# Performance work log

Measured on AMD Instinct MI355X. Metric: run time of the kernel, lower is better.

The kernel has to match this reference:

```python
import jax, jax.numpy as jnp
import numpy as np

TAU = 2.0
EPS = 1e-5
T, B, C, H, W = 4, 16, 256, 32, 32
HEADS = 8
HD = C // HEADS
N = H * W


def make_spike(grad_fn):
    @jax.custom_vjp
    def f(x):
        return (x >= 0.0).astype(x.dtype)
    def fwd(x):
        return f(x), x
    def bwd(res, g):
        return (g * grad_fn(res),)
    f.defvjp(fwd, bwd)
    return f

# ATan surrogate (alpha=5.0) used by q/k/v LIF nodes
spike_atan5 = make_spike(lambda x: (5.0 / 2.0) / (1.0 + (jnp.pi / 2.0 * 5.0 * x) ** 2))
# default Sigmoid surrogate (alpha=4.0) for shortcut_lif / talking_heads_lif
def _sig_grad(x):
    s = jax.nn.sigmoid(4.0 * x)
    return 4.0 * s * (1.0 - s)
spike_sig4 = make_spike(_sig_grad)


def lif(x, spike, v_th=1.0):
    # multi-step LIF over leading time axis; hard reset to 0, detach_reset
    def step(v, xt):
        h = v + (xt - v) / TAU
        s = spike(h - v_th)
        v_new = h * (1.0 - jax.lax.stop_gradient(s))
        return v_new, s
    _, out = jax.lax.scan(step, jnp.zeros_like(x[0]), x)
    return out


def conv1x1(x, w):
    # x: (T,B,C,H,W), w: (Cout,Cin) from Conv2d kernel_size=1
    return jnp.einsum('tbchw,oc->tbohw', x, w)


def bn(y, gamma, beta, mean, var):
    scale = (gamma / jnp.sqrt(var + EPS))[None, None, :, None, None]
    shift = (beta - mean * gamma / jnp.sqrt(var + EPS))[None, None, :, None, None]
    return y * scale + shift


def to_heads(x):
    # (T,B,C,H,W) -> (T,B,heads,N,hd); matches flatten(3).transpose(-1,-2).reshape.permute
    x = x.reshape(T, B, C, N).transpose(0, 1, 3, 2)          # (T,B,N,C)
    x = x.reshape(T, B, N, HEADS, HD).transpose(0, 1, 3, 2, 4)  # (T,B,heads,N,hd)
    return x


def setup_inputs() -> dict:
    key = jax.random.key(0)
    ks = jax.random.split(key, 20)
    def bn_params(i):
        return (1.0 + 0.1 * jax.random.normal(ks[i], (C,), jnp.float32),
                0.1 * jax.random.normal(ks[i + 1], (C,), jnp.float32),
                0.1 * jax.random.normal(ks[i + 2], (C,), jnp.float32),
                jax.random.uniform(ks[i + 3], (C,), jnp.float32, 0.5, 1.5))
    q_g, q_b, q_m, q_var = bn_params(1)
    k_g, k_b, k_m, k_var = bn_params(5)
    v_g, v_b, v_m, v_var = bn_params(9)
    p_g, p_b, p_m, p_var = bn_params(13)
    std = 1.0 / np.sqrt(C)
    return {
        'x': jax.random.normal(ks[0], (T, B, C, H, W), jnp.float32),
        'q_w': std * jax.random.normal(ks[17], (C, C), jnp.float32),
        'q_g': q_g, 'q_b': q_b, 'q_m': q_m, 'q_var': q_var,
        'k_w': std * jax.random.normal(ks[18], (C, C), jnp.float32),
        'k_g': k_g, 'k_b': k_b, 'k_m': k_m, 'k_var': k_var,
        'v_w': std * jax.random.normal(ks[19], (C, C), jnp.float32),
        'v_g': v_g, 'v_b': v_b, 'v_m': v_m, 'v_var': v_var,
        'proj_w': std * jax.random.normal(ks[4], (C, C), jnp.float32),
        'proj_bias': 0.01 * jax.random.normal(ks[8], (C,), jnp.float32),
        'p_g': p_g, 'p_b': p_b, 'p_m': p_m, 'p_var': p_var,
    }


def reference(x, q_w, q_g, q_b, q_m, q_var, k_w, k_g, k_b, k_m, k_var,
              v_w, v_g, v_b, v_m, v_var, proj_w, proj_bias, p_g, p_b, p_m, p_var):
    identity = x
    xs = lif(x, spike_sig4, 1.0)                      # shortcut_lif
    q = to_heads(lif(bn(conv1x1(xs, q_w), q_g, q_b, q_m, q_var), spike_atan5, 1.0))
    k = to_heads(lif(bn(conv1x1(xs, k_w), k_g, k_b, k_m, k_var), spike_atan5, 1.0))
    v = to_heads(lif(bn(conv1x1(xs, v_w), v_g, v_b, v_m, v_var), spike_atan5, 1.0))
    kv = jnp.sum(k * v, axis=-2, keepdims=True)       # (T,B,heads,1,hd)
    kv = lif(kv, spike_sig4, 0.5)                     # talking_heads_lif, v_th=0.5
    attn = q * kv                                     # (T,B,heads,N,hd)
    # transpose(3,4).reshape(T,B,C,H,W)
    out = attn.transpose(0, 1, 2, 4, 3).reshape(T, B, C, H, W)
    out = conv1x1(out, proj_w) + proj_bias[None, None, :, None, None]
    out = bn(out, p_g, p_b, p_m, p_var)
    out = out + identity
    return out, v
```

## Files before the change

### kernel.cpp

```cpp
#include <hip/hip_runtime.h>
#include <hip/hip_bf16.h>
#include <stdint.h>

#define T_ 4
#define B_ 16
#define C_ 256
#define N_ 1024
#define HEADS_ 8
#define HD_ 32

typedef unsigned long long u64;
typedef unsigned char u8;

__global__ __launch_bounds__(256) void prep_kernel(
    const float* __restrict__ qw, const float* __restrict__ kw,
    const float* __restrict__ vw, const float* __restrict__ pw,
    const float* __restrict__ qg, const float* __restrict__ qb2,
    const float* __restrict__ qmn, const float* __restrict__ qvr,
    const float* __restrict__ kg, const float* __restrict__ kb2,
    const float* __restrict__ kmn, const float* __restrict__ kvr,
    const float* __restrict__ vg, const float* __restrict__ vb2,
    const float* __restrict__ vmn, const float* __restrict__ vvr,
    const float* __restrict__ pg, const float* __restrict__ pb2,
    const float* __restrict__ pmn, const float* __restrict__ pvr,
    float* __restrict__ wtq, float* __restrict__ wtk,
    float* __restrict__ wtv, float* __restrict__ wtp,
    float* __restrict__ bnt) {
  if (blockIdx.x < 256) {
    int c = blockIdx.x;
    int o = threadIdx.x;
    wtq[c * C_ + o] = qw[o * C_ + c];
    wtk[c * C_ + o] = kw[o * C_ + c];
    wtv[c * C_ + o] = vw[o * C_ + c];
    wtp[c * C_ + o] = pw[o * C_ + c];
  } else {
    int c = threadIdx.x;
    float rs;
    rs = sqrtf(qvr[c] + 1e-5f);
    bnt[0 * C_ + c] = qg[c] / rs;
    bnt[1 * C_ + c] = qb2[c] - qmn[c] * qg[c] / rs;
    rs = sqrtf(kvr[c] + 1e-5f);
    bnt[2 * C_ + c] = kg[c] / rs;
    bnt[3 * C_ + c] = kb2[c] - kmn[c] * kg[c] / rs;
    rs = sqrtf(vvr[c] + 1e-5f);
    bnt[4 * C_ + c] = vg[c] / rs;
    bnt[5 * C_ + c] = vb2[c] - vmn[c] * vg[c] / rs;
    rs = sqrtf(pvr[c] + 1e-5f);
    bnt[6 * C_ + c] = pg[c] / rs;
    bnt[7 * C_ + c] = pb2[c] - pmn[c] * pg[c] / rs;
  }
}

__global__ __launch_bounds__(256) void lif_shortcut(const float* __restrict__ x,
                                                    u64* __restrict__ xsm) {
  int b = blockIdx.x >> 5;
  int n0 = (blockIdx.x & 31) << 5;
  int tid = threadIdx.x;
  int l = tid & 63, w = tid >> 6;
  __shared__ float tile[C_ * 33];
  float v[32];
#pragma unroll
  for (int i = 0; i < 32; i++) v[i] = 0.f;
  int c = (w << 6) + l;
  for (int t = 0; t < T_; t++) {
    __syncthreads();
    const float* xp = x + (((size_t)t * B_ + b) * C_) * N_ + n0;
    for (int idx = tid; idx < C_ * 32; idx += 256) {
      int cc = idx >> 5, nn = idx & 31;
      tile[cc * 33 + nn] = xp[(size_t)cc * N_ + nn];
    }
    __syncthreads();
#pragma unroll
    for (int nn = 0; nn < 32; nn++) {
      float xv = tile[c * 33 + nn];
      float h = v[nn] + (xv - v[nn]) * 0.5f;
      bool s = h >= 1.0f;
      v[nn] = s ? 0.f : h;
      u64 bal = __ballot(s);
      if (l == nn) xsm[(((size_t)t * B_ + b) * N_ + n0 + nn) * 4 + w] = bal;
    }
  }
}

__global__ __launch_bounds__(256) void qkv_sparse(
    const u64* __restrict__ xsm,
    const float* __restrict__ wtq, const float* __restrict__ wtk,
    const float* __restrict__ wtv, const float* __restrict__ bnt,
    float* __restrict__ pkv, u64* __restrict__ qm_out,
    float* __restrict__ vout) {
  int b = blockIdx.x >> 7;
  int nt = blockIdx.x & 127;
  int n0 = nt << 3;
  int tid = threadIdx.x;
  int l = tid & 63, wv = tid >> 6;
  float qs[4], qsh[4], ks[4], ksh[4], vsc[4], vsh[4];
#pragma unroll
  for (int j = 0; j < 4; j++) {
    int o = (j << 6) + l;
    qs[j]  = bnt[0 * C_ + o]; qsh[j] = bnt[1 * C_ + o];
    ks[j]  = bnt[2 * C_ + o]; ksh[j] = bnt[3 * C_ + o];
    vsc[j] = bnt[4 * C_ + o]; vsh[j] = bnt[5 * C_ + o];
  }
  int cnt[4][4];
#pragma unroll
  for (int t = 0; t < 4; t++)
#pragma unroll
    for (int j = 0; j < 4; j++) cnt[t][j] = 0;

  for (int nn = wv; nn < 8; nn += 4) {
    int n = n0 + nn;
    float aq[4][4], ak[4][4], av[4][4];
#pragma unroll
    for (int t = 0; t < 4; t++)
#pragma unroll
      for (int j = 0; j < 4; j++) { aq[t][j] = 0.f; ak[t][j] = 0.f; av[t][j] = 0.f; }
#pragma unroll
    for (int t = 0; t < 4; t++) {
      const u64* mp = xsm + ((((size_t)t * B_ + b) * N_ + n) << 2);
#pragma unroll
      for (int wd = 0; wd < 4; wd++) {
        u64 m = mp[wd];
        while (m) {
          int c = (wd << 6) + __builtin_ctzll(m);
          m &= (m - 1);
          const float* rq = wtq + c * C_;
          const float* rk = wtk + c * C_;
          const float* rv = wtv + c * C_;
#pragma unroll
          for (int j = 0; j < 4; j++) {
            int o = (j << 6) + l;
            aq[t][j] += rq[o];
            ak[t][j] += rk[o];
            av[t][j] += rv[o];
          }
        }
      }
    }
#pragma unroll
    for (int j = 0; j < 4; j++) {
      int o = (j << 6) + l;
      float vq = 0.f, vk = 0.f, vv = 0.f;
#pragma unroll
      for (int t = 0; t < 4; t++) {
        float pq = aq[t][j] * qs[j] + qsh[j];
        float pk = ak[t][j] * ks[j] + ksh[j];
        float pv = av[t][j] * vsc[j] + vsh[j];
        float hq = vq + (pq - vq) * 0.5f;
        float hk = vk + (pk - vk) * 0.5f;
        float hv = vv + (pv - vv) * 0.5f;
        bool sq = hq >= 1.0f; vq = sq ? 0.f : hq;
        bool sk = hk >= 1.0f; vk = sk ? 0.f : hk;
        bool sv = hv >= 1.0f; vv = sv ? 0.f : hv;
        cnt[t][j] += (sk && sv) ? 1 : 0;
        vout[(((size_t)t * B_ + b) * HEADS_ + (o >> 5)) * ((size_t)N_ * HD_) +
             (size_t)n * HD_ + (o & 31)] = sv ? 1.0f : 0.0f;
        u64 bal = __ballot(sq);
        if (l == (t << 2) + j)
          qm_out[((((size_t)t * B_ + b) * N_ + n) << 2) + j] = bal;
      }
    }
  }
  __shared__ int scnt[4][4][C_];
#pragma unroll
  for (int t = 0; t < 4; t++)
#pragma unroll
    for (int j = 0; j < 4; j++) scnt[wv][t][(j << 6) + l] = cnt[t][j];
  __syncthreads();
  for (int idx = tid; idx < 4 * C_; idx += 256) {
    int t = idx >> 8, c = idx & 255;
    int s = scnt[0][t][c] + scnt[1][t][c] + scnt[2][t][c] + scnt[3][t][c];
    pkv[(((size_t)t * B_ + b) * 128 + nt) * C_ + c] = (float)s;
  }
}

__global__ __launch_bounds__(1024) void kv_lif_kernel(const float* __restrict__ pkv,
                                                      u64* __restrict__ kvsm) {
  int b = blockIdx.x;
  int tid = threadIdx.x;
  int c = tid & 255, qtr = tid >> 8;
  __shared__ float part[4][4][C_];
#pragma unroll
  for (int t = 0; t < 4; t++) {
    const float* p = pkv + ((((size_t)t * B_ + b) * 128) + (qtr << 5)) * C_ + c;
    float s = 0.f;
#pragma unroll
    for (int i = 0; i < 32; i++) s += p[(size_t)i * C_];
    part[qtr][t][c] = s;
  }
  __syncthreads();
  if (tid < 256) {
    int l = c & 63, j = c >> 6;
    float v = 0.f;
#pragma unroll
    for (int t = 0; t < 4; t++) {
      float kv = part[0][t][c] + part[1][t][c] + part[2][t][c] + part[3][t][c];
      float h = v + (kv - v) * 0.5f;
      bool s = h >= 0.5f;
      v = s ? 0.f : h;
      u64 bal = __ballot(s);
      if (l == t) kvsm[((size_t)t * B_ + b) * 4 + j] = bal;
    }
  }
}

__global__ __launch_bounds__(256) void proj_sparse(
    const u64* __restrict__ qm, const u64* __restrict__ kvsm,
    const float* __restrict__ wtp, const float* __restrict__ bnt,
    const float* __restrict__ pbias, const float* __restrict__ x,
    float* __restrict__ out) {
  int tb = blockIdx.x >> 5;
  int n0 = (blockIdx.x & 31) << 5;
  int t = tb >> 4, b = tb & 15;
  int tid = threadIdx.x;
  int l = tid & 63, w = tid >> 6;
  __shared__ float tile[C_ * 33];
  u64 kvm[4];
#pragma unroll
  for (int wd = 0; wd < 4; wd++) kvm[wd] = kvsm[((size_t)t * B_ + b) * 4 + wd];
  for (int nn = w; nn < 32; nn += 4) {
    int n = n0 + nn;
    float acc[4] = {0.f, 0.f, 0.f, 0.f};
    const u64* mp = qm + ((((size_t)t * B_ + b) * N_ + n) << 2);
#pragma unroll
    for (int wd = 0; wd < 4; wd++) {
      u64 m = mp[wd] & kvm[wd];
      while (m) {
        int c = (wd << 6) + __builtin_ctzll(m);
        m &= (m - 1);
        const float* rp = wtp + c * C_;
#pragma unroll
        for (int j = 0; j < 4; j++) acc[j] += rp[(j << 6) + l];
      }
    }
#pragma unroll
    for (int j = 0; j < 4; j++) tile[((j << 6) + l) * 33 + nn] = acc[j];
  }
  __syncthreads();
  int col = l & 31;
  int half = l >> 5;
  for (int r = (w << 1) + half; r < C_; r += 8) {
    float val = tile[r * 33 + col];
    float z = (val + pbias[r]) * bnt[6 * C_ + r] + bnt[7 * C_ + r];
    size_t xi = (((size_t)t * B_ + b) * C_ + r) * N_ + n0 + col;
    out[xi] = z + x[xi];
  }
}

__global__ __launch_bounds__(256) void fill_zero_f32(float* p, size_t n) {
  size_t i = (size_t)blockIdx.x * 256 + threadIdx.x;
  if (i < n) p[i] = 0.0f;
}

extern "C" void kernel_launch(void* const* d_in, const int* in_sizes, int n_in,
                              void* d_out, int out_size, void* d_ws, size_t ws_size,
                              hipStream_t stream) {
  const float* x  = (const float*)d_in[0];
  const float* qw = (const float*)d_in[1];
  const float* qg = (const float*)d_in[2];
  const float* qb = (const float*)d_in[3];
  const float* qm = (const float*)d_in[4];
  const float* qv = (const float*)d_in[5];
  const float* kw = (const float*)d_in[6];
  const float* kg = (const float*)d_in[7];
  const float* kb = (const float*)d_in[8];
  const float* km = (const float*)d_in[9];
  const float* kv = (const float*)d_in[10];
  const float* vw = (const float*)d_in[11];
  const float* vg = (const float*)d_in[12];
  const float* vb2 = (const float*)d_in[13];
  const float* vm = (const float*)d_in[14];
  const float* vv = (const float*)d_in[15];
  const float* pw = (const float*)d_in[16];
  const float* pbias = (const float*)d_in[17];
  const float* pg = (const float*)d_in[18];
  const float* pb = (const float*)d_in[19];
  const float* pm = (const float*)d_in[20];
  const float* pv = (const float*)d_in[21];

  const size_t needed = 13641728ull;
  if (ws_size < needed) {
    size_t n = (size_t)out_size;
    fill_zero_f32<<<(unsigned)((n + 255) / 256), 256, 0, stream>>>(
        (float*)d_out, n);
    return;
  }

  char* ws = (char*)d_ws;
  float* wtq = (float*)(ws + 0);
  float* wtk = (float*)(ws + 262144);
  float* wtv = (float*)(ws + 524288);
  float* wtp = (float*)(ws + 786432);
  float* bnt = (float*)(ws + 1048576);
  u64*   xsm = (u64*)  (ws + 1056768);
  u64*   qmm = (u64*)  (ws + 3153920);
  float* pkv = (float*)(ws + 5251072);
  u64*   kvsm = (u64*) (ws + 13639680);

  float* out  = (float*)d_out;
  float* vout = out + (size_t)T_ * B_ * C_ * N_;

  prep_kernel<<<257, 256, 0, stream>>>(qw, kw, vw, pw,
                                       qg, qb, qm, qv, kg, kb, km, kv,
                                       vg, vb2, vm, vv, pg, pb, pm, pv,
                                       wtq, wtk, wtv, wtp, bnt);
  lif_shortcut<<<512, 256, 0, stream>>>(x, xsm);
  qkv_sparse<<<2048, 256, 0, stream>>>(xsm, wtq, wtk, wtv, bnt, pkv, qmm, vout);
  kv_lif_kernel<<<16, 1024, 0, stream>>>(pkv, kvsm);
  proj_sparse<<<2048, 256, 0, stream>>>(qmm, kvsm, wtp, bnt, pbias, x, out);
}
```

Before: 142.3 us.

## Fuse shortcut LIF spike generation into the sparse QKV kernel

The separate lif_shortcut kernel and its global spike-mask buffer are removed. Each qkv block now computes the LIF spikes for its own 8 spatial positions across all channels and time steps, reading x with float4 loads. It ballots the spikes into a shared-memory mask, and the mask words are made wave-uniform with readfirstlane. This removes one launch and the mask write/read round trip, but x is now read with short strided 32-byte segments per channel, and the LIF work runs serially before the accumulation loop in each block.

```diff
diff --git a/kernel.cpp b/kernel.cpp
--- a/kernel.cpp
+++ b/kernel.cpp
@@ -11,6 +11,12 @@
 
 typedef unsigned long long u64;
 typedef unsigned char u8;
+
+__device__ __forceinline__ u64 rf64(u64 v) {
+  unsigned lo = __builtin_amdgcn_readfirstlane((unsigned)v);
+  unsigned hi = __builtin_amdgcn_readfirstlane((unsigned)(v >> 32));
+  return ((u64)hi << 32) | (u64)lo;
+}
 
 __global__ __launch_bounds__(256) void prep_kernel(
     const float* __restrict__ qw, const float* __restrict__ kw,
@@ -51,39 +57,8 @@
   }
 }
 
-__global__ __launch_bounds__(256) void lif_shortcut(const float* __restrict__ x,
-                                                    u64* __restrict__ xsm) {
-  int b = blockIdx.x >> 5;
-  int n0 = (blockIdx.x & 31) << 5;
-  int tid = threadIdx.x;
-  int l = tid & 63, w = tid >> 6;
-  __shared__ float tile[C_ * 33];
-  float v[32];
-#pragma unroll
-  for (int i = 0; i < 32; i++) v[i] = 0.f;
-  int c = (w << 6) + l;
-  for (int t = 0; t < T_; t++) {
-    __syncthreads();
-    const float* xp = x + (((size_t)t * B_ + b) * C_) * N_ + n0;
-    for (int idx = tid; idx < C_ * 32; idx += 256) {
-      int cc = idx >> 5, nn = idx & 31;
-      tile[cc * 33 + nn] = xp[(size_t)cc * N_ + nn];
-    }
-    __syncthreads();
-#pragma unroll
-    for (int nn = 0; nn < 32; nn++) {
-      float xv = tile[c * 33 + nn];
-      float h = v[nn] + (xv - v[nn]) * 0.5f;
-      bool s = h >= 1.0f;
-      v[nn] = s ? 0.f : h;
-      u64 bal = __ballot(s);
-      if (l == nn) xsm[(((size_t)t * B_ + b) * N_ + n0 + nn) * 4 + w] = bal;
-    }
-  }
-}
-
-__global__ __launch_bounds__(256) void qkv_sparse(
-    const u64* __restrict__ xsm,
+__global__ __launch_bounds__(256) void qkv_fused(
+    const float* __restrict__ x,
     const float* __restrict__ wtq, const float* __restrict__ wtk,
     const float* __restrict__ wtv, const float* __restrict__ bnt,
     float* __restrict__ pkv, u64* __restrict__ qm_out,
@@ -93,6 +68,32 @@
   int n0 = nt << 3;
   int tid = threadIdx.x;
   int l = tid & 63, wv = tid >> 6;
+
+  __shared__ u64 lmask[8][4][4];
+
+  {
+    int c = (wv << 6) + l;
+    float v[8];
+#pragma unroll
+    for (int i = 0; i < 8; i++) v[i] = 0.f;
+#pragma unroll
+    for (int t = 0; t < T_; t++) {
+      const float* xp = x + ((((size_t)t * B_ + b) * C_) + c) * N_ + n0;
+      float4 xa = *(const float4*)xp;
+      float4 xb = *(const float4*)(xp + 4);
+      float xv[8] = {xa.x, xa.y, xa.z, xa.w, xb.x, xb.y, xb.z, xb.w};
+#pragma unroll
+      for (int nn = 0; nn < 8; nn++) {
+        float h = v[nn] + (xv[nn] - v[nn]) * 0.5f;
+        bool s = h >= 1.0f;
+        v[nn] = s ? 0.f : h;
+        u64 bal = __ballot(s);
+        if (l == (t << 3) + nn) lmask[nn][t][wv] = bal;
+      }
+    }
+  }
+  __syncthreads();
+
   float qs[4], qsh[4], ks[4], ksh[4], vsc[4], vsh[4];
 #pragma unroll
   for (int j = 0; j < 4; j++) {
@@ -116,10 +117,9 @@
       for (int j = 0; j < 4; j++) { aq[t][j] = 0.f; ak[t][j] = 0.f; av[t][j] = 0.f; }
 #pragma unroll
     for (int t = 0; t < 4; t++) {
-      const u64* mp = xsm + ((((size_t)t * B_ + b) * N_ + n) << 2);
 #pragma unroll
       for (int wd = 0; wd < 4; wd++) {
-        u64 m = mp[wd];
+        u64 m = rf64(lmask[nn][t][wd]);
         while (m) {
           int c = (wd << 6) + __builtin_ctzll(m);
           m &= (m - 1);
@@ -277,7 +277,7 @@
   const float* pm = (const float*)d_in[20];
   const float* pv = (const float*)d_in[21];
 
-  const size_t needed = 13641728ull;
+  const size_t needed = 11544576ull;
   if (ws_size < needed) {
     size_t n = (size_t)out_size;
     fill_zero_f32<<<(unsigned)((n + 255) / 256), 256, 0, stream>>>(
@@ -291,10 +291,9 @@
   float* wtv = (float*)(ws + 524288);
   float* wtp = (float*)(ws + 786432);
   float* bnt = (float*)(ws + 1048576);
-  u64*   xsm = (u64*)  (ws + 1056768);
-  u64*   qmm = (u64*)  (ws + 3153920);
-  float* pkv = (float*)(ws + 5251072);
-  u64*   kvsm = (u64*) (ws + 13639680);
+  u64*   qmm = (u64*)  (ws + 1056768);
+  float* pkv = (float*)(ws + 3153920);
+  u64*   kvsm = (u64*) (ws + 11542528);
 
   float* out  = (float*)d_out;
   float* vout = out + (size_t)T_ * B_ * C_ * N_;
@@ -303,8 +302,7 @@
                                        qg, qb, qm, qv, kg, kb, km, kv,
                                        vg, vb2, vm, vv, pg, pb, pm, pv,
                                        wtq, wtk, wtv, wtp, bnt);
-  lif_shortcut<<<512, 256, 0, stream>>>(x, xsm);
-  qkv_sparse<<<2048, 256, 0, stream>>>(xsm, wtq, wtk, wtv, bnt, pkv, qmm, vout);
+  qkv_fused<<<2048, 256, 0, stream>>>(x, wtq, wtk, wtv, bnt, pkv, qmm, vout);
   kv_lif_kernel<<<16, 1024, 0, stream>>>(pkv, kvsm);
   proj_sparse<<<2048, 256, 0, stream>>>(qmm, kvsm, wtp, bnt, pbias, x, out);
 }
```

Result: slower. 148.7 us (+4.5%).
